# Kernel tuning notes

Hardware: AMD Instinct MI355X
Metric: run time of the kernel (lower is better)

Reference implementation:

```python
import jax, jax.numpy as jnp
import numpy as np

HEADS = 16
DIM_HEAD = 64
BLOCK = 16
SEQ_LEN = 2048
NUM_BLOCKS = SEQ_LEN // BLOCK  # 128
NUM_RANDOM_BLOCKS = 32
LOCAL_WINDOW = 4
GLOBAL_BLOCKS = [0]


def make_layout():
    # Deterministic stand-in for DeepSpeed VariableSparsityConfig.make_layout
    # (local windows of 4 blocks + random blocks + global block columns/rows,
    #  then tril for unidirectional attention).
    rng = np.random.RandomState(0)
    nb = NUM_BLOCKS
    layout = np.zeros((nb, nb), dtype=bool)
    for w in range(0, nb, LOCAL_WINDOW):
        layout[w:w + LOCAL_WINDOW, w:w + LOCAL_WINDOW] = True
    rnd = rng.randint(0, nb, size=(nb, NUM_RANDOM_BLOCKS))
    layout[np.arange(nb)[:, None], rnd] = True
    for g in GLOBAL_BLOCKS:
        layout[:, g] = True
        layout[g, :] = True
    layout = np.tril(layout)  # unidirectional
    return jnp.asarray(layout)


def setup_inputs() -> dict:
    key = jax.random.key(0)
    k1, k2, k3 = jax.random.split(key, 3)
    dim = 1024
    inner = HEADS * DIM_HEAD  # 1024
    x = jax.random.normal(k1, (2, SEQ_LEN, dim), dtype=jnp.float32)
    w_qkv = jax.random.normal(k2, (dim, 3 * inner), dtype=jnp.float32) * 0.02
    w_out = jax.random.normal(k3, (inner, dim), dtype=jnp.float32) * 0.02
    b_out = jnp.zeros((dim,), dtype=jnp.float32)
    layout = make_layout()  # [128, 128] bool
    return {"x": x, "w_qkv": w_qkv, "w_out": w_out, "b_out": b_out, "layout": layout}


def reference(x, w_qkv, w_out, b_out, layout):
    b, n, _ = x.shape
    scale = DIM_HEAD ** -0.5
    qkv = x @ w_qkv  # [b, n, 3*h*d]
    q, k, v = jnp.split(qkv, 3, axis=-1)
    split_heads = lambda t: t.reshape(b, n, HEADS, DIM_HEAD).transpose(0, 2, 1, 3)
    q, k, v = split_heads(q), split_heads(k), split_heads(v)  # [b, h, n, d]

    scores = jnp.einsum('bhid,bhjd->bhij', q, k) * scale  # [b, h, n, n]
    neg = -jnp.finfo(scores.dtype).max
    # additive causal attn_mask (value = -finfo.max / 2, attn_mask_mode='add')
    causal = jnp.triu(jnp.ones((n, n), dtype=bool), 1)
    scores = scores + jnp.where(causal, neg / 2, jnp.zeros((), scores.dtype))
    # block-sparse layout: entries outside allowed blocks are fully masked
    allowed = jnp.repeat(jnp.repeat(layout, BLOCK, axis=0), BLOCK, axis=1)  # [n, n]
    scores = jnp.where(allowed, scores, neg)
    attn = jax.nn.softmax(scores, axis=-1)
    out = jnp.einsum('bhij,bhjd->bhid', attn, v)  # [b, h, n, d]
    out = out.transpose(0, 2, 1, 3).reshape(b, n, HEADS * DIM_HEAD)
    return out @ w_out + b_out
```

## Files before the change

kernel.cpp:

```cpp
#include <hip/hip_runtime.h>
#include <cstdint>
#include <cstddef>


typedef short bf8 __attribute__((ext_vector_type(8)));
typedef float f32x4 __attribute__((ext_vector_type(4)));
typedef unsigned short u16;
typedef unsigned int u32;

#define MFMA_BF16(a, b, c) __builtin_amdgcn_mfma_f32_16x16x32_bf16((a), (b), (c), 0, 0, 0)

constexpr int SEQ = 2048;
constexpr int NH = 16;
constexpr int DHD = 64;
constexpr int NBLK = 128;
constexpr int DIM = 1024;

__device__ __forceinline__ u32 pack2bf(float a, float b) {
  u32 r;
  asm("v_cvt_pk_bf16_f32 %0, %1, %2" : "=v"(r) : "v"(a), "v"(b));
  return r;
}
__device__ __forceinline__ void gload_lds16(const u16* g, u16* l) {
  auto gp = (const __attribute__((address_space(1))) u16*)(g);
  auto lp = (__attribute__((address_space(3))) u16*)(l);
  __builtin_amdgcn_global_load_lds(gp, lp, 16, 0, 0);
}

__global__ __launch_bounds__(256) void prep(
    const float* __restrict__ x, u16* __restrict__ xbf,
    const float* __restrict__ wqkv, u16* __restrict__ wqkvT,
    const float* __restrict__ wout, u16* __restrict__ woutT,
    const unsigned char* __restrict__ lay,
    int* __restrict__ cnt, int* __restrict__ cols) {
  __shared__ u16 tile[64][72];
  int bid = blockIdx.x;
  int t = threadIdx.x;

  if (bid < 2048) {
    int idx = (bid * 256 + t) * 8;
    float4 a = *(const float4*)(x + idx);
    float4 b = *(const float4*)(x + idx + 4);
    *(uint4*)(xbf + idx) = make_uint4(pack2bf(a.x, a.y), pack2bf(a.z, a.w),
                                      pack2bf(b.x, b.y), pack2bf(b.z, b.w));
    return;
  }
  bid -= 2048;
  if (bid < 768 + 256) {
    const float* in; u16* out; int C, bx, by;
    if (bid < 768) { in = wqkv; out = wqkvT; C = 3072; bx = bid % 48; by = bid / 48; }
    else { int r = bid - 768; in = wout; out = woutT; C = 1024; bx = r % 16; by = r / 16; }
    const int R = 1024;
    int c0 = bx * 64, r0 = by * 64;
    int rr = t >> 4, cc = (t & 15) * 4;
    #pragma unroll
    for (int p = 0; p < 64; p += 16) {
      float4 v = *(const float4*)(in + (size_t)(r0 + rr + p) * C + c0 + cc);
      *(u32*)&tile[rr + p][cc + 0] = pack2bf(v.x, v.y);
      *(u32*)&tile[rr + p][cc + 2] = pack2bf(v.z, v.w);
    }
    __syncthreads();
    int oc = t >> 3, orr = (t & 7) * 8;
    #pragma unroll
    for (int p = 0; p < 64; p += 32) {
      u16 tmp[8];
      #pragma unroll
      for (int qy = 0; qy < 8; qy++) tmp[qy] = tile[orr + qy][oc + p];
      u16* dst = out + (size_t)(c0 + oc + p) * R + r0 + orr;
      *(ushort4*)(dst)     = make_ushort4(tmp[0], tmp[1], tmp[2], tmp[3]);
      *(ushort4*)(dst + 4) = make_ushort4(tmp[4], tmp[5], tmp[6], tmp[7]);
    }
    return;
  }
  bid -= 1024;
  int wave = t >> 6, lane = t & 63;
  int i = bid * 4 + wave;
  const uint4* l4 = (const uint4*)lay;
  u32 acc = 0;
  #pragma unroll
  for (int it = 0; it < 16; it++) {
    uint4 v = l4[it * 64 + lane];
    acc |= ((v.x | v.y | v.z | v.w) & 0xFFFFFF00u);
  }
  bool as_int32 = (__ballot(acc != 0) == 0ULL);
  const int* li = (const int*)lay;
  int j0 = lane, j1 = lane + 64;
  bool p0 = (j0 <= i) && (as_int32 ? (li[i * 128 + j0] != 0) : (lay[i * 128 + j0] != 0));
  bool p1 = (j1 <= i) && (as_int32 ? (li[i * 128 + j1] != 0) : (lay[i * 128 + j1] != 0));
  unsigned long long m0 = __ballot(p0), m1 = __ballot(p1);
  unsigned long long lt = (1ULL << lane) - 1ULL;
  int base0 = __popcll(m0);
  if (p0) cols[i * 128 + __popcll(m0 & lt)] = j0;
  if (p1) cols[i * 128 + base0 + __popcll(m1 & lt)] = j1;
  if (lane == 0) cnt[i] = base0 + __popcll(m1);
}

__global__ __launch_bounds__(256) void gemm_qkv(
    const u16* __restrict__ A, const u16* __restrict__ Bt,
    u16* __restrict__ oq, u16* __restrict__ okk, u16* __restrict__ ov) {
  __shared__ u16 smem[16896];
  u16* bA0 = smem;
  u16* bB0 = smem + 4096;
  u16* bA1 = smem + 8192;
  u16* bB1 = smem + 12288;
  const int K = 1024;
  int tid = threadIdx.x, lane = tid & 63, wave = tid >> 6;
  int quad = lane >> 4, l16 = lane & 15;
  int wr = wave >> 1, wc = wave & 1;
  int d = blockIdx.x;
  int xcd = d & 7, rest = d >> 3;
  int bm = xcd + (rest & 3) * 8;
  int bn = rest >> 2;
  int bm0 = bm * 128, bn0 = bn * 128;

  f32x4 acc[4][4];
  #pragma unroll
  for (int i = 0; i < 4; i++)
    #pragma unroll
    for (int j = 0; j < 4; j++) acc[i][j] = (f32x4){0.f, 0.f, 0.f, 0.f};

  int srow = lane >> 2;
  int schunk = ((lane & 3) ^ (srow & 3)) * 8;
  int phys = (quad ^ (l16 & 3)) * 8;

  auto stage = [&](u16* dA, u16* dB, int k0) {
    #pragma unroll
    for (int r = 0; r < 2; r++) {
      int row = wave * 32 + r * 16;
      gload_lds16(A  + (size_t)(bm0 + row + srow) * K + k0 + schunk, dA + row * 32);
      gload_lds16(Bt + (size_t)(bn0 + row + srow) * K + k0 + schunk, dB + row * 32);
    }
  };
  auto compute = [&](const u16* cA, const u16* cB) {
    bf8 af[4], bfr[4];
    #pragma unroll
    for (int i = 0; i < 4; i++)
      af[i] = *(const bf8*)(cA + (wr * 64 + i * 16 + l16) * 32 + phys);
    #pragma unroll
    for (int j = 0; j < 4; j++)
      bfr[j] = *(const bf8*)(cB + (wc * 64 + j * 16 + l16) * 32 + phys);
    #pragma unroll
    for (int i = 0; i < 4; i++)
      #pragma unroll
      for (int j = 0; j < 4; j++)
        acc[i][j] = MFMA_BF16(af[i], bfr[j], acc[i][j]);
  };

  stage(bA0, bB0, 0);
  for (int k0 = 0; k0 < K; k0 += 64) {
    __syncthreads();
    if (k0 + 32 < K) stage(bA1, bB1, k0 + 32);
    compute(bA0, bB0);
    __syncthreads();
    if (k0 + 64 < K) stage(bA0, bB0, k0 + 64);
    compute(bA1, bB1);
  }

  int which = bn0 >> 10;
  if (which == 2) {
    #pragma unroll
    for (int j = 0; j < 4; j++) {
      int c = bn0 + wc * 64 + j * 16 + l16;
      int h = (c & 1023) >> 6, dd = c & 63;
      #pragma unroll
      for (int i = 0; i < 4; i++) {
        int r0 = bm0 + wr * 64 + i * 16;
        int b = r0 >> 11, nn0 = r0 & 2047, jb = nn0 >> 4;
        u16* dst = ov + ((size_t)((b * NH + h) * NBLK + jb) * DHD + dd) * 16 + quad * 4;
        *(uint2*)dst = make_uint2(pack2bf(acc[i][j][0], acc[i][j][1]),
                                  pack2bf(acc[i][j][2], acc[i][j][3]));
      }
    }
  } else {
    u16* dstbase = (which == 0) ? oq : okk;
    float m = (which == 0) ? 0.18033688f : 1.0f;
    __syncthreads();
    #pragma unroll
    for (int j = 0; j < 4; j++) {
      int col = wc * 64 + j * 16 + l16;
      #pragma unroll
      for (int i = 0; i < 4; i++) {
        int row = wr * 64 + i * 16 + quad * 4;
        *(uint2*)&smem[col * 132 + row] =
            make_uint2(pack2bf(acc[i][j][0] * m, acc[i][j][1] * m),
                       pack2bf(acc[i][j][2] * m, acc[i][j][3] * m));
      }
    }
    __syncthreads();
    int r = tid >> 1, half = tid & 1;
    int rglob = bm0 + r;
    int b = rglob >> 11, nn = rglob & 2047;
    int h = ((bn0 & 1023) >> 6) + half;
    #pragma unroll
    for (int j = 0; j < 4; j++) {
      union { u16 t[16]; uint4 q[2]; } tv;
      #pragma unroll
      for (int dd = 0; dd < 16; dd++)
        tv.t[dd] = smem[(half * 64 + j * 16 + dd) * 132 + r];
      u16* dst = dstbase + ((size_t)(b * NH + h) * SEQ + nn) * DHD + j * 16;
      *(uint4*)(dst) = tv.q[0];
      *(uint4*)(dst + 8) = tv.q[1];
    }
  }
}

__global__ __launch_bounds__(256) void gemm_out(
    const u16* __restrict__ A, const u16* __restrict__ Bt,
    float* __restrict__ of, const float* __restrict__ bias) {
  __shared__ u16 smem[12288];
  u16* bA0 = smem;
  u16* bB0 = smem + 4096;
  u16* bA1 = smem + 6144;
  u16* bB1 = smem + 10240;
  const int K = 1024, N = 1024;
  int tid = threadIdx.x, lane = tid & 63, wave = tid >> 6;
  int quad = lane >> 4, l16 = lane & 15;
  int wr = wave >> 1, wc = wave & 1;
  int d = blockIdx.x;
  int xcd = d & 7, slot = d >> 3;
  int bm = xcd * 4 + (slot & 3);
  int bn = slot >> 2;
  int bm0 = bm * 128, bn0 = bn * 64;

  f32x4 acc[4][2];
  #pragma unroll
  for (int i = 0; i < 4; i++)
    #pragma unroll
    for (int j = 0; j < 2; j++) acc[i][j] = (f32x4){0.f, 0.f, 0.f, 0.f};

  int srow = lane >> 2;
  int schunk = ((lane & 3) ^ (srow & 3)) * 8;
  int phys = (quad ^ (l16 & 3)) * 8;

  auto stage = [&](u16* dA, u16* dB, int k0) {
    #pragma unroll
    for (int r = 0; r < 2; r++) {
      int row = wave * 32 + r * 16;
      gload_lds16(A + (size_t)(bm0 + row + srow) * K + k0 + schunk, dA + row * 32);
    }
    int brow = wave * 16;
    gload_lds16(Bt + (size_t)(bn0 + brow + srow) * K + k0 + schunk, dB + brow * 32);
  };
  auto compute = [&](const u16* cA, const u16* cB) {
    bf8 af[4], bfr[2];
    #pragma unroll
    for (int i = 0; i < 4; i++)
      af[i] = *(const bf8*)(cA + (wr * 64 + i * 16 + l16) * 32 + phys);
    #pragma unroll
    for (int j = 0; j < 2; j++)
      bfr[j] = *(const bf8*)(cB + (wc * 32 + j * 16 + l16) * 32 + phys);
    #pragma unroll
    for (int i = 0; i < 4; i++)
      #pragma unroll
      for (int j = 0; j < 2; j++)
        acc[i][j] = MFMA_BF16(af[i], bfr[j], acc[i][j]);
  };

  stage(bA0, bB0, 0);
  for (int k0 = 0; k0 < K; k0 += 64) {
    __syncthreads();
    if (k0 + 32 < K) stage(bA1, bB1, k0 + 32);
    compute(bA0, bB0);
    __syncthreads();
    if (k0 + 64 < K) stage(bA0, bB0, k0 + 64);
    compute(bA1, bB1);
  }

  #pragma unroll
  for (int j = 0; j < 2; j++) {
    int c = bn0 + wc * 32 + j * 16 + l16;
    float bv = bias[c];
    #pragma unroll
    for (int i = 0; i < 4; i++) {
      int rbase = bm0 + wr * 64 + i * 16 + quad * 4;
      #pragma unroll
      for (int ii = 0; ii < 4; ii++)
        of[(size_t)(rbase + ii) * N + c] = acc[i][j][ii] + bv;
    }
  }
}

__global__ __launch_bounds__(256) void attn_sparse(
    const u16* __restrict__ q, const u16* __restrict__ k, const u16* __restrict__ vblk,
    const int* __restrict__ cnt, const int* __restrict__ cols,
    u16* __restrict__ aout) {
  int wave = threadIdx.x >> 6, lane = threadIdx.x & 63;
  int quad = lane >> 4, l16 = lane & 15;
  int blk = blockIdx.x;
  int xcd = blk & 7, rest = blk >> 3;
  int bh = xcd * 4 + (rest & 3);
  int strip = rest >> 2;
  int qb = 127 - (strip * 4 + wave);

  const u16* qp = q + ((size_t)bh * SEQ + qb * 16) * DHD + l16 * DHD + quad * 8;
  bf8 qa0 = *(const bf8*)(qp);
  bf8 qa1 = *(const bf8*)(qp + 32);

  float l_i = 0.f;
  f32x4 o[4];
  #pragma unroll
  for (int t = 0; t < 4; t++) o[t] = (f32x4){0.f, 0.f, 0.f, 0.f};

  int count = cnt[qb];
  const int* mc = cols + qb * NBLK;

  bf8 bufA[8], bufB[8];
  int jA0 = 0, jA1 = 0, jB0 = 0, jB1 = 0;
  bool hA = false, hB = false;

  auto ldpair = [&](int p, bf8* kv, int& o0, int& o1, bool& ohv) {
    o0 = mc[p];
    ohv = (p + 1 < count);
    o1 = ohv ? mc[p + 1] : o0;
    const u16* kp0 = k + ((size_t)bh * SEQ + o0 * 16) * DHD + l16 * DHD + quad * 8;
    kv[0] = *(const bf8*)(kp0); kv[1] = *(const bf8*)(kp0 + 32);
    const u16* kp1 = k + ((size_t)bh * SEQ + o1 * 16) * DHD + l16 * DHD + quad * 8;
    kv[2] = *(const bf8*)(kp1); kv[3] = *(const bf8*)(kp1 + 32);
    int jq = (quad < 2) ? o0 : o1;
    const u16* vp = vblk + (size_t)(bh * NBLK + jq) * 1024 + l16 * 16 + (quad & 1) * 8;
    kv[4] = *(const bf8*)(vp);
    kv[5] = *(const bf8*)(vp + 256);
    kv[6] = *(const bf8*)(vp + 512);
    kv[7] = *(const bf8*)(vp + 768);
  };

  auto process = [&](const bf8* buf, int j0, int j1, bool hv) {
    __builtin_amdgcn_s_setprio(1);
    f32x4 S0 = (f32x4){0.f, 0.f, 0.f, 0.f};
    S0 = MFMA_BF16(buf[0], qa0, S0);
    S0 = MFMA_BF16(buf[1], qa1, S0);
    f32x4 S1 = (f32x4){0.f, 0.f, 0.f, 0.f};
    S1 = MFMA_BF16(buf[2], qa0, S1);
    S1 = MFMA_BF16(buf[3], qa1, S1);
    __builtin_amdgcn_s_setprio(0);

    float e0[4], e1[4];
    #pragma unroll
    for (int r = 0; r < 4; r++) {
      int kl = quad * 4 + r;
      float s0 = S0[r];
      if (j0 == qb && kl > l16) s0 = -1e38f;
      float s1 = hv ? S1[r] : -1e38f;
      if (hv && j1 == qb && kl > l16) s1 = -1e38f;
      e0[r] = exp2f(s0);
      e1[r] = exp2f(s1);
      l_i += e0[r] + e1[r];
    }

    u32 a0 = pack2bf(e0[0], e0[1]);
    u32 a1 = pack2bf(e0[2], e0[3]);
    u32 a2 = pack2bf(e1[0], e1[1]);
    u32 a3 = pack2bf(e1[2], e1[3]);
    asm("v_permlane32_swap_b32 %0, %1" : "+v"(a0), "+v"(a2));
    asm("v_permlane32_swap_b32 %0, %1" : "+v"(a1), "+v"(a3));
    asm("v_permlane16_swap_b32 %0, %1" : "+v"(a0), "+v"(a2));
    asm("v_permlane16_swap_b32 %0, %1" : "+v"(a1), "+v"(a3));
    union { uint4 w; bf8 v; } pf;
    pf.w = make_uint4(a0, a1, a2, a3);

    __builtin_amdgcn_s_setprio(1);
    o[0] = MFMA_BF16(buf[4], pf.v, o[0]);
    o[1] = MFMA_BF16(buf[5], pf.v, o[1]);
    o[2] = MFMA_BF16(buf[6], pf.v, o[2]);
    o[3] = MFMA_BF16(buf[7], pf.v, o[3]);
    __builtin_amdgcn_s_setprio(0);
  };

  ldpair(0, bufA, jA0, jA1, hA);
  if (2 < count) ldpair(2, bufB, jB0, jB1, hB);

  for (int p = 0; p < count; p += 4) {
    process(bufA, jA0, jA1, hA);
    if (p + 4 < count) ldpair(p + 4, bufA, jA0, jA1, hA);
    if (p + 2 < count) process(bufB, jB0, jB1, hB);
    if (p + 6 < count) ldpair(p + 6, bufB, jB0, jB1, hB);
  }

  float l = l_i;
  l += __shfl_xor(l, 16);
  l += __shfl_xor(l, 32);
  float inv = 1.0f / l;
  int b = bh >> 4, h = bh & 15;
  int n = qb * 16 + l16;
  u16* dst = aout + ((size_t)b * SEQ + n) * DIM + h * DHD;
  #pragma unroll
  for (int t = 0; t < 4; t++) {
    *(uint2*)(dst + t * 16 + quad * 4) =
        make_uint2(pack2bf(o[t][0] * inv, o[t][1] * inv),
                   pack2bf(o[t][2] * inv, o[t][3] * inv));
  }
}

extern "C" void kernel_launch(void* const* d_in, const int* in_sizes, int n_in,
                              void* d_out, int out_size, void* d_ws, size_t ws_size,
                              hipStream_t stream) {
  const float* x      = (const float*)d_in[0];
  const float* w_qkv  = (const float*)d_in[1];
  const float* w_out  = (const float*)d_in[2];
  const float* b_out  = (const float*)d_in[3];
  const unsigned char* layout = (const unsigned char*)d_in[4];
  float* out = (float*)d_out;

  char* ws = (char*)d_ws;
  u16* xbf   = (u16*)(ws);
  u16* wqkvT = (u16*)(ws + (8u  << 20));
  u16* woutT = (u16*)(ws + (14u << 20) + (512u << 10));
  u16* qB    = (u16*)(ws + (17u << 20));
  u16* kB    = (u16*)(ws + (25u << 20));
  u16* vblk  = (u16*)(ws + (33u << 20));
  u16* aout  = (u16*)(ws + (41u << 20));
  int* cnt   = (int*)(ws + (49u << 20));
  int* cols  = (int*)(ws + (49u << 20) + 4096);

  prep<<<3104, 256, 0, stream>>>(x, xbf, w_qkv, wqkvT, w_out, woutT,
                                 layout, cnt, cols);
  gemm_qkv<<<768, 256, 0, stream>>>(xbf, wqkvT, qB, kB, vblk);
  attn_sparse<<<1024, 256, 0, stream>>>(qB, kB, vblk, cnt, cols, aout);
  gemm_out<<<512, 256, 0, stream>>>(aout, woutT, out, b_out);
}
```

Before: 169.3 us.

## Triple-buffer QKV GEMM LDS staging with explicit vmcnt waits and setprio

```diff
diff --git a/kernel.cpp b/kernel.cpp
--- a/kernel.cpp
+++ b/kernel.cpp
@@ -98,11 +98,7 @@
 __global__ __launch_bounds__(256) void gemm_qkv(
     const u16* __restrict__ A, const u16* __restrict__ Bt,
     u16* __restrict__ oq, u16* __restrict__ okk, u16* __restrict__ ov) {
-  __shared__ u16 smem[16896];
-  u16* bA0 = smem;
-  u16* bB0 = smem + 4096;
-  u16* bA1 = smem + 8192;
-  u16* bB1 = smem + 12288;
+  __shared__ u16 smem[24576];
   const int K = 1024;
   int tid = threadIdx.x, lane = tid & 63, wave = tid >> 6;
   int quad = lane >> 4, l16 = lane & 15;
@@ -131,29 +127,45 @@
       gload_lds16(Bt + (size_t)(bn0 + row + srow) * K + k0 + schunk, dB + row * 32);
     }
   };
-  auto compute = [&](const u16* cA, const u16* cB) {
+
+  u16* b0A = smem;          u16* b0B = smem + 4096;
+  u16* b1A = smem + 8192;   u16* b1B = smem + 12288;
+  u16* b2A = smem + 16384;  u16* b2B = smem + 20480;
+
+  stage(b0A, b0B, 0);
+  stage(b1A, b1B, 32);
+  asm volatile("s_waitcnt vmcnt(4)" ::: "memory");
+  __builtin_amdgcn_s_barrier();
+
+  for (int p = 0; p < 32; ++p) {
+    int k2 = (p + 2) * 32;
+    if (k2 < K) stage(b2A, b2B, k2);
+
     bf8 af[4], bfr[4];
     #pragma unroll
     for (int i = 0; i < 4; i++)
-      af[i] = *(const bf8*)(cA + (wr * 64 + i * 16 + l16) * 32 + phys);
+      af[i] = *(const bf8*)(b0A + (wr * 64 + i * 16 + l16) * 32 + phys);
     #pragma unroll
     for (int j = 0; j < 4; j++)
-      bfr[j] = *(const bf8*)(cB + (wc * 64 + j * 16 + l16) * 32 + phys);
+      bfr[j] = *(const bf8*)(b0B + (wc * 64 + j * 16 + l16) * 32 + phys);
+
+    if (k2 < K)       asm volatile("s_waitcnt vmcnt(4)" ::: "memory");
+    else if (p == 30) asm volatile("s_waitcnt vmcnt(0)" ::: "memory");
+
+    __builtin_amdgcn_s_setprio(1);
     #pragma unroll
     for (int i = 0; i < 4; i++)
       #pragma unroll
       for (int j = 0; j < 4; j++)
         acc[i][j] = MFMA_BF16(af[i], bfr[j], acc[i][j]);
-  };
-
-  stage(bA0, bB0, 0);
-  for (int k0 = 0; k0 < K; k0 += 64) {
-    __syncthreads();
-    if (k0 + 32 < K) stage(bA1, bB1, k0 + 32);
-    compute(bA0, bB0);
-    __syncthreads();
-    if (k0 + 64 < K) stage(bA0, bB0, k0 + 64);
-    compute(bA1, bB1);
+    __builtin_amdgcn_s_setprio(0);
+
+    __builtin_amdgcn_s_barrier();
+
+    u16* tA = b0A; u16* tB = b0B;
+    b0A = b1A; b0B = b1B;
+    b1A = b2A; b1B = b2B;
+    b2A = tA;  b2B = tB;
   }
 
   int which = bn0 >> 10;
```

Result: no change. 169.1 us (-0.1%).

## Enlarge QKV GEMM tile to 256x256 with 8-wave interleaved pipelined schedule

Applied to the files above, without the earlier changes.

```diff
diff --git a/kernel.cpp b/kernel.cpp
--- a/kernel.cpp
+++ b/kernel.cpp
@@ -95,111 +95,178 @@
   if (lane == 0) cnt[i] = base0 + __popcll(m1);
 }
 
-__global__ __launch_bounds__(256) void gemm_qkv(
+__global__ __launch_bounds__(512, 2) void gemm_qkv(
     const u16* __restrict__ A, const u16* __restrict__ Bt,
     u16* __restrict__ oq, u16* __restrict__ okk, u16* __restrict__ ov) {
-  __shared__ u16 smem[16896];
-  u16* bA0 = smem;
-  u16* bB0 = smem + 4096;
-  u16* bA1 = smem + 8192;
-  u16* bB1 = smem + 12288;
+  __shared__ u16 smem[65536];
   const int K = 1024;
   int tid = threadIdx.x, lane = tid & 63, wave = tid >> 6;
   int quad = lane >> 4, l16 = lane & 15;
-  int wr = wave >> 1, wc = wave & 1;
+  int wr = wave >> 2, wc = wave & 3;
   int d = blockIdx.x;
   int xcd = d & 7, rest = d >> 3;
-  int bm = xcd + (rest & 3) * 8;
-  int bn = rest >> 2;
-  int bm0 = bm * 128, bn0 = bn * 128;
-
-  f32x4 acc[4][4];
-  #pragma unroll
-  for (int i = 0; i < 4; i++)
+  int bn = rest % 12;
+  int bm = xcd + (rest / 12) * 8;
+  int bm0 = bm * 256, bn0 = bn * 256;
+
+  f32x4 acc[8][4];
+  #pragma unroll
+  for (int i = 0; i < 8; i++)
     #pragma unroll
     for (int j = 0; j < 4; j++) acc[i][j] = (f32x4){0.f, 0.f, 0.f, 0.f};
 
-  int srow = lane >> 2;
-  int schunk = ((lane & 3) ^ (srow & 3)) * 8;
-  int phys = (quad ^ (l16 & 3)) * 8;
-
-  auto stage = [&](u16* dA, u16* dB, int k0) {
-    #pragma unroll
-    for (int r = 0; r < 2; r++) {
-      int row = wave * 32 + r * 16;
-      gload_lds16(A  + (size_t)(bm0 + row + srow) * K + k0 + schunk, dA + row * 32);
-      gload_lds16(Bt + (size_t)(bn0 + row + srow) * K + k0 + schunk, dB + row * 32);
-    }
-  };
-  auto compute = [&](const u16* cA, const u16* cB) {
-    bf8 af[4], bfr[4];
-    #pragma unroll
-    for (int i = 0; i < 4; i++)
-      af[i] = *(const bf8*)(cA + (wr * 64 + i * 16 + l16) * 32 + phys);
-    #pragma unroll
-    for (int j = 0; j < 4; j++)
-      bfr[j] = *(const bf8*)(cB + (wc * 64 + j * 16 + l16) * 32 + phys);
-    #pragma unroll
-    for (int i = 0; i < 4; i++)
-      #pragma unroll
-      for (int j = 0; j < 4; j++)
-        acc[i][j] = MFMA_BF16(af[i], bfr[j], acc[i][j]);
-  };
-
-  stage(bA0, bB0, 0);
-  for (int k0 = 0; k0 < K; k0 += 64) {
-    __syncthreads();
-    if (k0 + 32 < K) stage(bA1, bB1, k0 + 32);
-    compute(bA0, bB0);
-    __syncthreads();
-    if (k0 + 64 < K) stage(bA0, bB0, k0 + 64);
-    compute(bA1, bB1);
-  }
-
+  int tgl = ((l16 >> 2) & 1) << 1;
+  int aBase = wr * 8192;
+  int bBase = 32768 + (wc >> 1) * 8192;
+  int bRow0 = (wc & 1) * 64;
+
+  auto ldA = [&](int db, int rf, int kk) -> bf8 {
+    int idx = db * 16384 + aBase + (rf * 16 + l16) * 64 + ((kk * 4 + quad) ^ tgl) * 8;
+    return *(const bf8*)(smem + idx);
+  };
+  auto ldB = [&](int db, int cf, int kk) -> bf8 {
+    int idx = db * 16384 + bBase + (bRow0 + cf * 16 + l16) * 64 + ((kk * 4 + quad) ^ tgl) * 8;
+    return *(const bf8*)(smem + idx);
+  };
+
+  auto stageA = [&](int db, int k0) {
+    #pragma unroll
+    for (int h = 0; h < 2; h++)
+      #pragma unroll
+      for (int i = 0; i < 2; i++) {
+        int slot = i * 512 + tid;
+        int row = slot >> 3;
+        int c = (slot & 7) ^ (((row >> 2) & 1) << 1);
+        gload_lds16(A + (size_t)(bm0 + h * 128 + row) * K + k0 + c * 8,
+                    smem + db * 16384 + h * 8192 + (i * 512 + wave * 64) * 8);
+      }
+  };
+  auto stageB = [&](int db, int k0) {
+    #pragma unroll
+    for (int h = 0; h < 2; h++)
+      #pragma unroll
+      for (int i = 0; i < 2; i++) {
+        int slot = i * 512 + tid;
+        int row = slot >> 3;
+        int c = (slot & 7) ^ (((row >> 2) & 1) << 1);
+        gload_lds16(Bt + (size_t)(bn0 + h * 128 + row) * K + k0 + c * 8,
+                    smem + 32768 + db * 16384 + h * 8192 + (i * 512 + wave * 64) * 8);
+      }
+  };
+
+  bf8 Ab[4][2], Bb[4][2];
+  auto LDA = [&](int db, int rbase) {
+    #pragma unroll
+    for (int r = 0; r < 4; r++)
+      #pragma unroll
+      for (int kk = 0; kk < 2; kk++) Ab[r][kk] = ldA(db, rbase + r, kk);
+  };
+  auto LDB = [&](int db, int clo) {
+    #pragma unroll
+    for (int c = 0; c < 2; c++)
+      #pragma unroll
+      for (int kk = 0; kk < 2; kk++) Bb[clo + c][kk] = ldB(db, clo + c, kk);
+  };
+  auto MF = [&](int rbase, int clo) {
+    __builtin_amdgcn_s_setprio(1);
+    #pragma unroll
+    for (int r = 0; r < 4; r++)
+      #pragma unroll
+      for (int c = 0; c < 2; c++)
+        #pragma unroll
+        for (int kk = 0; kk < 2; kk++)
+          acc[rbase + r][clo + c] =
+              MFMA_BF16(Ab[r][kk], Bb[clo + c][kk], acc[rbase + r][clo + c]);
+    __builtin_amdgcn_s_setprio(0);
+  };
+  auto BAR = [&]() { __builtin_amdgcn_s_barrier(); };
+
+  stageA(0, 0); stageB(0, 0); stageA(1, 64);
+  asm volatile("s_waitcnt vmcnt(4)" ::: "memory");
+  BAR();
+
+  for (int i = 0; i < 8; ++i) {
+    int kc = i * 128;
+    LDA(0, 0); LDB(0, 0);
+    stageB(1, kc + 64);
+    BAR(); MF(0, 0); BAR();
+    LDB(0, 2);
+    BAR(); MF(0, 2); BAR();
+    LDA(0, 4);
+    BAR(); MF(4, 2); BAR();
+    if (i < 7) {
+      stageA(0, kc + 128);
+      asm volatile("s_waitcnt vmcnt(4)" ::: "memory");
+    } else {
+      asm volatile("s_waitcnt vmcnt(0)" ::: "memory");
+    }
+    BAR(); MF(4, 0); BAR();
+    LDA(1, 0); LDB(1, 0);
+    if (i < 7) stageB(0, kc + 128);
+    BAR(); MF(0, 0); BAR();
+    LDB(1, 2);
+    BAR(); MF(0, 2); BAR();
+    LDA(1, 4);
+    BAR(); MF(4, 2); BAR();
+    if (i < 7) {
+      stageA(1, kc + 192);
+      asm volatile("s_waitcnt vmcnt(4)" ::: "memory");
+    }
+    BAR(); MF(4, 0); BAR();
+  }
+
+  __syncthreads();
   int which = bn0 >> 10;
   if (which == 2) {
     #pragma unroll
-    for (int j = 0; j < 4; j++) {
-      int c = bn0 + wc * 64 + j * 16 + l16;
+    for (int cf = 0; cf < 4; cf++) {
+      int c = bn0 + wc * 64 + cf * 16 + l16;
       int h = (c & 1023) >> 6, dd = c & 63;
       #pragma unroll
-      for (int i = 0; i < 4; i++) {
-        int r0 = bm0 + wr * 64 + i * 16;
+      for (int rf = 0; rf < 8; rf++) {
+        int r0 = bm0 + wr * 128 + rf * 16;
         int b = r0 >> 11, nn0 = r0 & 2047, jb = nn0 >> 4;
         u16* dst = ov + ((size_t)((b * NH + h) * NBLK + jb) * DHD + dd) * 16 + quad * 4;
-        *(uint2*)dst = make_uint2(pack2bf(acc[i][j][0], acc[i][j][1]),
-                                  pack2bf(acc[i][j][2], acc[i][j][3]));
+        *(uint2*)dst = make_uint2(pack2bf(acc[rf][cf][0], acc[rf][cf][1]),
+                                  pack2bf(acc[rf][cf][2], acc[rf][cf][3]));
       }
     }
   } else {
     u16* dstbase = (which == 0) ? oq : okk;
     float m = (which == 0) ? 0.18033688f : 1.0f;
-    __syncthreads();
-    #pragma unroll
-    for (int j = 0; j < 4; j++) {
-      int col = wc * 64 + j * 16 + l16;
-      #pragma unroll
-      for (int i = 0; i < 4; i++) {
-        int row = wr * 64 + i * 16 + quad * 4;
-        *(uint2*)&smem[col * 132 + row] =
-            make_uint2(pack2bf(acc[i][j][0] * m, acc[i][j][1] * m),
-                       pack2bf(acc[i][j][2] * m, acc[i][j][3] * m));
+    #pragma unroll
+    for (int ph = 0; ph < 2; ph++) {
+      if ((wc >> 1) == ph) {
+        #pragma unroll
+        for (int cf = 0; cf < 4; cf++) {
+          int lcol = (wc & 1) * 64 + cf * 16 + l16;
+          #pragma unroll
+          for (int rf = 0; rf < 8; rf++) {
+            int row = wr * 128 + rf * 16 + quad * 4;
+            *(uint2*)&smem[lcol * 260 + row] =
+                make_uint2(pack2bf(acc[rf][cf][0] * m, acc[rf][cf][1] * m),
+                           pack2bf(acc[rf][cf][2] * m, acc[rf][cf][3] * m));
+          }
+        }
       }
-    }
-    __syncthreads();
-    int r = tid >> 1, half = tid & 1;
-    int rglob = bm0 + r;
-    int b = rglob >> 11, nn = rglob & 2047;
-    int h = ((bn0 & 1023) >> 6) + half;
-    #pragma unroll
-    for (int j = 0; j < 4; j++) {
-      union { u16 t[16]; uint4 q[2]; } tv;
-      #pragma unroll
-      for (int dd = 0; dd < 16; dd++)
-        tv.t[dd] = smem[(half * 64 + j * 16 + dd) * 132 + r];
-      u16* dst = dstbase + ((size_t)(b * NH + h) * SEQ + nn) * DHD + j * 16;
-      *(uint4*)(dst) = tv.q[0];
-      *(uint4*)(dst + 8) = tv.q[1];
+      __syncthreads();
+      {
+        int r = tid >> 1, half = tid & 1;
+        int rglob = bm0 + r;
+        int b = rglob >> 11, nn = rglob & 2047;
+        int h = (((bn0 + ph * 128) & 1023) >> 6) + half;
+        #pragma unroll
+        for (int j = 0; j < 4; j++) {
+          union { u16 t[16]; uint4 q[2]; } tv;
+          #pragma unroll
+          for (int dd = 0; dd < 16; dd++)
+            tv.t[dd] = smem[(half * 64 + j * 16 + dd) * 260 + r];
+          u16* dst = dstbase + ((size_t)(b * NH + h) * SEQ + nn) * DHD + j * 16;
+          *(uint4*)(dst) = tv.q[0];
+          *(uint4*)(dst + 8) = tv.q[1];
+        }
+      }
+      __syncthreads();
     }
   }
 }
@@ -414,7 +481,7 @@
 
   prep<<<3104, 256, 0, stream>>>(x, xbf, w_qkv, wqkvT, w_out, woutT,
                                  layout, cnt, cols);
-  gemm_qkv<<<768, 256, 0, stream>>>(xbf, wqkvT, qB, kB, vblk);
+  gemm_qkv<<<192, 512, 0, stream>>>(xbf, wqkvT, qB, kB, vblk);
   attn_sparse<<<1024, 256, 0, stream>>>(qB, kB, vblk, cnt, cols, aout);
   gemm_out<<<512, 256, 0, stream>>>(aout, woutT, out, b_out);
 }
```

Result: slower. 179.9 us (+6.3%).
